# Performance work log

Hardware: AMD Instinct MI355X
Metric: run time of the kernel (lower is better)

## Reference

```python
import jax, jax.numpy as jnp
import numpy as np

B, S, V = 8, 512, 32000

def setup_inputs() -> dict:
    key = jax.random.key(0)
    k1, k2, k3 = jax.random.split(key, 3)
    predict = jax.random.normal(k1, (B, S, V), dtype=jnp.float32)
    target = jax.random.randint(k2, (B, S), 0, V, dtype=jnp.int64)
    # word lengths in [1, S] so every example has at least one valid token
    mask = jax.random.randint(k3, (B, 1), 1, S + 1, dtype=jnp.int64)
    return {"predict": predict, "target": target, "mask": mask}

def reference(predict, target, mask):
    # predict: [B, S, V], target: [B, S], mask: [B, 1] with mask[:,0] = word_len
    logp = jax.nn.log_softmax(predict, axis=-1)                       # [B, S, V]
    tok_nll = -jnp.take_along_axis(logp, target[..., None], axis=-1)[..., 0]  # [B, S]
    word_len = mask[:, 0]                                             # [B]
    valid = (jnp.arange(predict.shape[1])[None, :] < word_len[:, None])       # [B, S]
    per_example = jnp.sum(tok_nll * valid, axis=1) / word_len.astype(tok_nll.dtype)  # mean over first word_len tokens
    return jnp.mean(per_example)
```

## Files before the change

kernel.cpp:

```cpp
#include <hip/hip_runtime.h>
#include <math.h>

#define BB 8
#define SS 512
#define VV 32000
#define NV4 (VV / 4)

__global__ __launch_bounds__(256) void masked_ce_kernel(
    const float* __restrict__ predict,
    const int*   __restrict__ target,
    const int*   __restrict__ mask,
    float*       __restrict__ out)
{
    const int row = blockIdx.x;
    const int b   = row >> 9;
    const int s   = row & 511;
    const int wl  = mask[b];
    if (s >= wl) return;

    const float* rowp = predict + (size_t)row * VV;
    const float4* rp4 = (const float4*)rowp;
    const int tid = threadIdx.x;

    float s0 = 0.0f, s1 = 0.0f;
    int i = tid;
    for (; i + 256 < NV4; i += 512) {
        float4 a = rp4[i];
        float4 c = rp4[i + 256];
        s0 += __expf(a.x) + __expf(a.y) + __expf(a.z) + __expf(a.w);
        s1 += __expf(c.x) + __expf(c.y) + __expf(c.z) + __expf(c.w);
    }
    if (i < NV4) {
        float4 a = rp4[i];
        s0 += __expf(a.x) + __expf(a.y) + __expf(a.z) + __expf(a.w);
    }
    float sum = s0 + s1;

    #pragma unroll
    for (int off = 32; off > 0; off >>= 1)
        sum += __shfl_down(sum, off, 64);

    __shared__ float ssum[4];
    const int wave = tid >> 6;
    if ((tid & 63) == 0) ssum[wave] = sum;
    __syncthreads();

    if (tid == 0) {
        float Sv = ssum[0] + ssum[1] + ssum[2] + ssum[3];
        const int t   = target[row];
        const float xt = rowp[t];
        const float nll = __logf(Sv) - xt;
        atomicAdd(out, nll / ((float)wl * (float)BB));
    }
}

extern "C" void kernel_launch(void* const* d_in, const int* in_sizes, int n_in,
                              void* d_out, int out_size, void* d_ws, size_t ws_size,
                              hipStream_t stream) {
    const float* predict = (const float*)d_in[0];
    const int*   target  = (const int*)  d_in[1];
    const int*   mask    = (const int*)  d_in[2];
    float* out = (float*)d_out;

    hipMemsetAsync(out, 0, sizeof(float), stream);

    masked_ce_kernel<<<BB * SS, 256, 0, stream>>>(predict, target, mask, out);
}
```

Before: 626.8 us.

## Split each row into four chunk blocks with a separate finalize reduction kernel

Each vocab row is split across four blocks, and each block loads all eight float4 chunks per thread up front before exponentiating, so more loads are in flight at once. Partial sums go to workspace, and a single-block finalize kernel combines the chunks, gathers target logits, and reduces the loss deterministically. This replaces the atomicAdd and memset, at the cost of an extra kernel launch and a serial single-block tail.

```diff
diff --git a/kernel.cpp b/kernel.cpp
--- a/kernel.cpp
+++ b/kernel.cpp
@@ -4,54 +4,92 @@
 #define BB 8
 #define SS 512
 #define VV 32000
-#define NV4 (VV / 4)
+#define ROWS (BB * SS)
+#define CHUNKS 4
+#define CF4 2000
 
-__global__ __launch_bounds__(256) void masked_ce_kernel(
+__global__ __launch_bounds__(256) void chunk_sumexp_kernel(
     const float* __restrict__ predict,
-    const int*   __restrict__ target,
     const int*   __restrict__ mask,
-    float*       __restrict__ out)
+    float*       __restrict__ ws)
 {
-    const int row = blockIdx.x;
-    const int b   = row >> 9;
-    const int s   = row & 511;
-    const int wl  = mask[b];
-    if (s >= wl) return;
+    const int bid   = blockIdx.x;
+    const int row   = bid >> 2;
+    const int chunk = bid & 3;
+    const int b     = row >> 9;
+    const int s     = row & 511;
+    if (s >= mask[b]) return;
 
-    const float* rowp = predict + (size_t)row * VV;
-    const float4* rp4 = (const float4*)rowp;
+    const float4* rp4 = (const float4*)(predict + (size_t)row * VV) + (size_t)chunk * CF4;
     const int tid = threadIdx.x;
 
-    float s0 = 0.0f, s1 = 0.0f;
-    int i = tid;
-    for (; i + 256 < NV4; i += 512) {
-        float4 a = rp4[i];
-        float4 c = rp4[i + 256];
-        s0 += __expf(a.x) + __expf(a.y) + __expf(a.z) + __expf(a.w);
-        s1 += __expf(c.x) + __expf(c.y) + __expf(c.z) + __expf(c.w);
+    float4 v0 = rp4[tid];
+    float4 v1 = rp4[tid + 256];
+    float4 v2 = rp4[tid + 512];
+    float4 v3 = rp4[tid + 768];
+    float4 v4 = rp4[tid + 1024];
+    float4 v5 = rp4[tid + 1280];
+    float4 v6 = rp4[tid + 1536];
+    float s7 = 0.0f;
+    if (tid < CF4 - 7 * 256) {
+        float4 v7 = rp4[tid + 1792];
+        s7 = __expf(v7.x) + __expf(v7.y) + __expf(v7.z) + __expf(v7.w);
     }
-    if (i < NV4) {
-        float4 a = rp4[i];
-        s0 += __expf(a.x) + __expf(a.y) + __expf(a.z) + __expf(a.w);
-    }
-    float sum = s0 + s1;
+
+    float sum = s7
+        + __expf(v0.x) + __expf(v0.y) + __expf(v0.z) + __expf(v0.w)
+        + __expf(v1.x) + __expf(v1.y) + __expf(v1.z) + __expf(v1.w)
+        + __expf(v2.x) + __expf(v2.y) + __expf(v2.z) + __expf(v2.w)
+        + __expf(v3.x) + __expf(v3.y) + __expf(v3.z) + __expf(v3.w)
+        + __expf(v4.x) + __expf(v4.y) + __expf(v4.z) + __expf(v4.w)
+        + __expf(v5.x) + __expf(v5.y) + __expf(v5.z) + __expf(v5.w)
+        + __expf(v6.x) + __expf(v6.y) + __expf(v6.z) + __expf(v6.w);
 
     #pragma unroll
     for (int off = 32; off > 0; off >>= 1)
         sum += __shfl_down(sum, off, 64);
 
     __shared__ float ssum[4];
-    const int wave = tid >> 6;
-    if ((tid & 63) == 0) ssum[wave] = sum;
+    if ((tid & 63) == 0) ssum[tid >> 6] = sum;
     __syncthreads();
+    if (tid == 0)
+        ws[bid] = ssum[0] + ssum[1] + ssum[2] + ssum[3];
+}
 
-    if (tid == 0) {
-        float Sv = ssum[0] + ssum[1] + ssum[2] + ssum[3];
-        const int t   = target[row];
-        const float xt = rowp[t];
-        const float nll = __logf(Sv) - xt;
-        atomicAdd(out, nll / ((float)wl * (float)BB));
+__global__ __launch_bounds__(256) void finalize_kernel(
+    const float* __restrict__ predict,
+    const int*   __restrict__ target,
+    const int*   __restrict__ mask,
+    const float* __restrict__ ws,
+    float*       __restrict__ out)
+{
+    const int tid = threadIdx.x;
+    float acc = 0.0f;
+
+    #pragma unroll
+    for (int k = 0; k < ROWS / 256; ++k) {
+        const int r  = tid + k * 256;
+        const int b  = r >> 9;
+        const int s  = r & 511;
+        const int wl = mask[b];
+        if (s < wl) {
+            const float4 p = ((const float4*)ws)[r];
+            const float  S = (p.x + p.y) + (p.z + p.w);
+            const int    t = target[r];
+            const float xt = predict[(size_t)r * VV + t];
+            acc += (__logf(S) - xt) / ((float)wl * (float)BB);
+        }
     }
+
+    #pragma unroll
+    for (int off = 32; off > 0; off >>= 1)
+        acc += __shfl_down(acc, off, 64);
+
+    __shared__ float ssum[4];
+    if ((tid & 63) == 0) ssum[tid >> 6] = acc;
+    __syncthreads();
+    if (tid == 0)
+        out[0] = ssum[0] + ssum[1] + ssum[2] + ssum[3];
 }
 
 extern "C" void kernel_launch(void* const* d_in, const int* in_sizes, int n_in,
@@ -61,8 +99,8 @@
     const int*   target  = (const int*)  d_in[1];
     const int*   mask    = (const int*)  d_in[2];
     float* out = (float*)d_out;
+    float* ws  = (float*)d_ws;
 
-    hipMemsetAsync(out, 0, sizeof(float), stream);
-
-    masked_ce_kernel<<<BB * SS, 256, 0, stream>>>(predict, target, mask, out);
+    chunk_sumexp_kernel<<<ROWS * CHUNKS, 256, 0, stream>>>(predict, mask, ws);
+    finalize_kernel<<<1, 256, 0, stream>>>(predict, target, mask, ws, out);
 }
```

Measured after the change: 623.2 us. No clear change (-0.6%).
